# Performance work log

Hardware: AMD Instinct MI355X
Metric: run time of the kernel (lower is better)

The kernel has to match this reference:

```python
import jax, jax.numpy as jnp
import numpy as np

B, N, D, H, W, C = 2, 4, 48, 28, 60, 64
DOWNSAMPLE = 8
NX, NY, NZ = 192, 192, 1   # from size=(192,192), scale=0.25; zbound=[-10,10,20] -> nz=1
SCALE = 0.25
OFFSETX = 0
DMIN, DMAX, DSTEP = 2.0, 50.0, 1.0


def setup_inputs() -> dict:
    key = jax.random.key(0)
    x = jax.random.normal(key, (B, N, D, H, W, C), dtype=jnp.float32)
    ogfW, ogfH = W * DOWNSAMPLE, H * DOWNSAMPLE
    fx = fy = 250.0
    K = jnp.array([[fx, 0.0, ogfW / 2.0], [0.0, fy, ogfH / 2.0], [0.0, 0.0, 1.0]], jnp.float32)
    intrinsics = jnp.broadcast_to(K, (B, N, 3, 3))
    # camera->ego rotation: cam z (forward) -> ego x, cam x (right) -> ego -y, cam y (down) -> ego -z
    R = jnp.array([[0.0, 0.0, 1.0], [-1.0, 0.0, 0.0], [0.0, -1.0, 0.0]], jnp.float32)
    pose = jnp.zeros((B, N, 4, 4), jnp.float32)
    pose = pose.at[..., :3, :3].set(R)
    pose = pose.at[..., :3, 3].set(jnp.array([1.0, 0.0, 1.6], jnp.float32))
    pose = pose.at[..., 3, 3].set(1.0)
    return {"x": x, "intrinsics": intrinsics, "pose": pose}


def _frustum():
    # (D,H,W,3) frustum of (u*d, v*d, d) homogeneous pixel coords scaled by depth
    ds = jnp.arange(DMIN, DMAX, DSTEP, dtype=jnp.float32)          # (D,)
    xs = jnp.linspace(0.0, W * DOWNSAMPLE - 1, W, dtype=jnp.float32)
    ys = jnp.linspace(0.0, H * DOWNSAMPLE - 1, H, dtype=jnp.float32)
    d = jnp.broadcast_to(ds[:, None, None], (D, H, W))
    u = jnp.broadcast_to(xs[None, None, :], (D, H, W))
    v = jnp.broadcast_to(ys[None, :, None], (D, H, W))
    return jnp.stack([u * d, v * d, d], axis=-1)


def reference(x, intrinsics, pose):
    rots = pose[..., :3, :3]                 # (B,N,3,3)
    trans = pose[..., :3, 3]                 # (B,N,3)
    pts = _frustum()                         # (D,H,W,3)
    combine = rots @ jnp.linalg.inv(intrinsics)  # (B,N,3,3)
    # ego-frame point cloud: (B,N,D,H,W,3)
    geom = jnp.einsum('bnij,dhwj->bndhwi', combine, pts) + trans[:, :, None, None, None, :]
    # bev_intrinsics from bev_params_to_intrinsics(size, scale, offsetx)
    f_bev = 1.0 / SCALE
    cx_bev = NX / 2.0 + OFFSETX
    cy_bev = NY / 2.0
    # torch .long() truncates toward zero, same as astype(int32)
    gx = (geom[..., 0] * f_bev + cx_bev).astype(jnp.int32)
    gy = (geom[..., 1] * f_bev + cy_bev).astype(jnp.int32)
    gz = ((geom[..., 2] + 10.0) / 20.0).astype(jnp.int32)  # (z - bx2 + dx2/2)/dx2, bx2=0, dx2=20
    b = jnp.broadcast_to(jnp.arange(B, dtype=jnp.int32)[:, None, None, None, None], gx.shape)
    kept = (gx >= 0) & (gx < NX) & (gy >= 0) & (gy < NY) & (gz >= 0) & (gz < NZ)
    # segment scatter-add == sort + cumsum-diff + scatter-set (ranks unique after reduction)
    flat = ((b * NZ + gz) * NY + gy) * NX + gx
    flat = jnp.where(kept, flat, 0).reshape(-1)
    xf = jnp.where(kept[..., None], x, jnp.zeros((), x.dtype)).reshape(-1, C)
    out = jnp.zeros((B * NZ * NY * NX, C), x.dtype).at[flat].add(xf)
    out = out.reshape(B, NZ, NY, NX, C)
    # final[b, :, z, y, x] layout then cat(unbind(dim=2), dim=1) -> (B, NZ*C, NY, NX)
    return out.transpose(0, 1, 4, 2, 3).reshape(B, NZ * C, NY, NX)
```

## Files before the change

kernel.cpp:

```cpp
#include <hip/hip_runtime.h>

#define BB 2
#define NN 4
#define DD 48
#define HH 28
#define WW 60
#define CC 64
#define NXg 192
#define NYg 192
#define NZg 1
#define DOWNS 8

constexpr int PTS    = BB * NN * DD * HH * WW;
constexpr int NCELLS = BB * NZg * NYg * NXg;
constexpr int NYX    = NYg * NXg;

__global__ void setup_kernel(const float* __restrict__ intr,
                             const float* __restrict__ pose,
                             double* __restrict__ coef) {
    int i = threadIdx.x;
    if (i >= BB * NN) return;
    const float* K  = intr + (size_t)i * 9;
    const float* Pm = pose + (size_t)i * 16;

    double k00 = K[0], k01 = K[1], k02 = K[2];
    double k10 = K[3], k11 = K[4], k12 = K[5];
    double k20 = K[6], k21 = K[7], k22 = K[8];

    double det = k00 * (k11 * k22 - k12 * k21)
               - k01 * (k10 * k22 - k12 * k20)
               + k02 * (k10 * k21 - k11 * k20);
    double id = 1.0 / det;
    double i00 = (k11 * k22 - k12 * k21) * id;
    double i01 = (k02 * k21 - k01 * k22) * id;
    double i02 = (k01 * k12 - k02 * k11) * id;
    double i10 = (k12 * k20 - k10 * k22) * id;
    double i11 = (k00 * k22 - k02 * k20) * id;
    double i12 = (k02 * k10 - k00 * k12) * id;
    double i20 = (k10 * k21 - k11 * k20) * id;
    double i21 = (k01 * k20 - k00 * k21) * id;
    double i22 = (k00 * k11 - k01 * k10) * id;

    double r00 = Pm[0],  r01 = Pm[1],  r02 = Pm[2],  tx = Pm[3];
    double r10 = Pm[4],  r11 = Pm[5],  r12 = Pm[6],  ty = Pm[7];
    double r20 = Pm[8],  r21 = Pm[9],  r22 = Pm[10], tz = Pm[11];

    double* c = coef + (size_t)i * 12;
    c[0] = r00 * i00 + r01 * i10 + r02 * i20;
    c[1] = r00 * i01 + r01 * i11 + r02 * i21;
    c[2] = r00 * i02 + r01 * i12 + r02 * i22;
    c[3] = r10 * i00 + r11 * i10 + r12 * i20;
    c[4] = r10 * i01 + r11 * i11 + r12 * i21;
    c[5] = r10 * i02 + r11 * i12 + r12 * i22;
    c[6] = r20 * i00 + r21 * i10 + r22 * i20;
    c[7] = r20 * i01 + r21 * i11 + r22 * i21;
    c[8] = r20 * i02 + r21 * i12 + r22 * i22;
    c[9]  = tx;
    c[10] = ty;
    c[11] = tz;
}

__global__ void __launch_bounds__(256)
scatter_kernel(const float* __restrict__ x,
               const double* __restrict__ coef,
               float* __restrict__ outT) {
    int tid  = threadIdx.x;
    int lane = tid & 63;
    int p    = blockIdx.x * 256 + tid;

    int w  = p % WW;
    int t  = p / WW;
    int h  = t % HH; t /= HH;
    int d  = t % DD;
    int bn = t / DD;
    int b  = bn / NN;

    const double* cf = coef + (size_t)bn * 12;

    double u   = (double)w * ((double)(WW * DOWNS - 1) / (double)(WW - 1));
    double v   = (double)h * ((double)(HH * DOWNS - 1) / (double)(HH - 1));
    double dep = 2.0 + (double)d;

    double rx = cf[0] * u + cf[1] * v + cf[2];
    double ry = cf[3] * u + cf[4] * v + cf[5];
    double rz = cf[6] * u + cf[7] * v + cf[8];

    double gxf = (rx * dep + cf[9])  * 4.0 + 96.0;
    double gyf = (ry * dep + cf[10]) * 4.0 + 96.0;
    double gzf = ((rz * dep + cf[11]) + 10.0) / 20.0;

    int gx = (int)gxf;
    int gy = (int)gyf;
    int gz = (int)gzf;

    bool kept = (gx >= 0) & (gx < NXg) & (gy >= 0) & (gy < NYg) &
                (gz >= 0) & (gz < NZg);

    int cell = kept ? (((b * NZg + gz) * NYg + gy) * NXg + gx) : -1;

    unsigned long long mask = __ballot(cell >= 0);
    if (mask == 0ULL) return;

    int base = p - lane;
    float acc = 0.f;
    int   cur = -1;

    while (mask) {
        int k[8], c[8];
        #pragma unroll
        for (int j = 0; j < 8; ++j) {
            k[j] = __ffsll((long long)mask) - 1;
            mask &= mask - 1ULL;
        }
        #pragma unroll
        for (int j = 0; j < 8; ++j) {
            int kj = k[j] >= 0 ? k[j] : 0;
            int cj = __shfl(cell, kj);
            c[j] = k[j] >= 0 ? cj : -1;
        }
        float val[8];
        #pragma unroll
        for (int j = 0; j < 8; ++j) {
            int kj = k[j] >= 0 ? k[j] : 0;
            val[j] = x[(size_t)(base + kj) * CC + lane];
        }
        #pragma unroll
        for (int j = 0; j < 8; ++j) {
            if (c[j] < 0) continue;
            if (c[j] == cur) {
                acc += val[j];
            } else {
                if (cur >= 0) atomicAdd(&outT[(size_t)cur * CC + lane], acc);
                cur = c[j];
                acc = val[j];
            }
        }
    }
    if (cur >= 0) atomicAdd(&outT[(size_t)cur * CC + lane], acc);
}

__global__ void __launch_bounds__(256)
transpose_kernel(const float* __restrict__ outT,
                 float* __restrict__ out) {
    __shared__ float tile[64][65];
    int tid      = threadIdx.x;
    int cellbase = blockIdx.x * 64;

    const float* src = outT + (size_t)cellbase * CC;
    #pragma unroll
    for (int i = 0; i < 16; ++i) {
        int idx = i * 256 + tid;
        tile[idx >> 6][idx & 63] = src[idx];
    }
    __syncthreads();

    int bb     = cellbase / NYX;
    int yxbase = cellbase % NYX;
    float* dst = out + (size_t)bb * CC * NYX + yxbase;
    #pragma unroll
    for (int i = 0; i < 16; ++i) {
        int idx = i * 256 + tid;
        int ch  = idx >> 6;
        int cl  = idx & 63;
        dst[(size_t)ch * NYX + cl] = tile[cl][ch];
    }
}

extern "C" void kernel_launch(void* const* d_in, const int* in_sizes, int n_in,
                              void* d_out, int out_size, void* d_ws, size_t ws_size,
                              hipStream_t stream) {
    const float* x    = (const float*)d_in[0];
    const float* intr = (const float*)d_in[1];
    const float* pose = (const float*)d_in[2];
    float* out = (float*)d_out;

    double* coef = (double*)d_ws;
    float*  outT = (float*)d_ws + 256;

    hipMemsetAsync(outT, 0, (size_t)NCELLS * CC * sizeof(float), stream);
    setup_kernel<<<1, 64, 0, stream>>>(intr, pose, coef);
    scatter_kernel<<<PTS / 256, 256, 0, stream>>>(x, coef, outT);
    transpose_kernel<<<NCELLS / 64, 256, 0, stream>>>(outT, out);
}
```

Before: 270.6 us.

## Remap scatter so each wave reduces a full (b,d,w) column across cameras and rows

Result: faster. 229.2 us (-15.3%).

```diff
diff --git a/kernel.cpp b/kernel.cpp
--- a/kernel.cpp
+++ b/kernel.cpp
@@ -11,9 +11,10 @@
 #define NZg 1
 #define DOWNS 8
 
-constexpr int PTS    = BB * NN * DD * HH * WW;
+constexpr int DHW    = DD * HH * WW;
 constexpr int NCELLS = BB * NZg * NYg * NXg;
 constexpr int NYX    = NYg * NXg;
+constexpr int GWAVES = BB * DD * WW;
 
 __global__ void setup_kernel(const float* __restrict__ intr,
                              const float* __restrict__ pose,
@@ -66,73 +67,96 @@
                float* __restrict__ outT) {
     int tid  = threadIdx.x;
     int lane = tid & 63;
-    int p    = blockIdx.x * 256 + tid;
-
-    int w  = p % WW;
-    int t  = p / WW;
-    int h  = t % HH; t /= HH;
-    int d  = t % DD;
-    int bn = t / DD;
-    int b  = bn / NN;
-
-    const double* cf = coef + (size_t)bn * 12;
+    int gw   = blockIdx.x * 4 + (tid >> 6);
+
+    int w = gw % WW;
+    int t = gw / WW;
+    int d = t % DD;
+    int b = t / DD;
 
     double u   = (double)w * ((double)(WW * DOWNS - 1) / (double)(WW - 1));
-    double v   = (double)h * ((double)(HH * DOWNS - 1) / (double)(HH - 1));
     double dep = 2.0 + (double)d;
-
-    double rx = cf[0] * u + cf[1] * v + cf[2];
-    double ry = cf[3] * u + cf[4] * v + cf[5];
-    double rz = cf[6] * u + cf[7] * v + cf[8];
-
-    double gxf = (rx * dep + cf[9])  * 4.0 + 96.0;
-    double gyf = (ry * dep + cf[10]) * 4.0 + 96.0;
-    double gzf = ((rz * dep + cf[11]) + 10.0) / 20.0;
-
-    int gx = (int)gxf;
-    int gy = (int)gyf;
-    int gz = (int)gzf;
-
-    bool kept = (gx >= 0) & (gx < NXg) & (gy >= 0) & (gy < NYg) &
-                (gz >= 0) & (gz < NZg);
-
-    int cell = kept ? (((b * NZg + gz) * NYg + gy) * NXg + gx) : -1;
-
-    unsigned long long mask = __ballot(cell >= 0);
-    if (mask == 0ULL) return;
-
-    int base = p - lane;
+    const double vstep = (double)(HH * DOWNS - 1) / (double)(HH - 1);
+
+    int    cellv[4];
+    double Az[4], Bz[4];
+    bool   fastok = true;
+    #pragma unroll
+    for (int n = 0; n < NN; ++n) {
+        const double* cf = coef + (size_t)(b * NN + n) * 12;
+        double Bx = cf[1] * dep * 4.0;
+        double By = cf[4] * dep * 4.0;
+        if (Bx != 0.0 || By != 0.0) fastok = false;
+        double gxf = ((cf[0] * u + cf[2]) * dep + cf[9])  * 4.0 + 96.0;
+        double gyf = ((cf[3] * u + cf[5]) * dep + cf[10]) * 4.0 + 96.0;
+        int gx = (int)gxf;
+        int gy = (int)gyf;
+        bool kxy = (gx >= 0) & (gx < NXg) & (gy >= 0) & (gy < NYg);
+        cellv[n] = kxy ? ((b * NZg + 0) * NYg + gy) * NXg + gx : -1;
+        Az[n] = ((cf[6] * u + cf[8]) * dep + cf[11] + 10.0) / 20.0;
+        Bz[n] = cf[7] * dep * vstep / 20.0;
+    }
+    bool same = (cellv[0] == cellv[1]) & (cellv[1] == cellv[2]) &
+                (cellv[2] == cellv[3]);
+
+    unsigned hm[4];
+    #pragma unroll
+    for (int n = 0; n < NN; ++n) {
+        unsigned m = 0;
+        #pragma unroll
+        for (int h = 0; h < HH; ++h) {
+            double zf = Az[n] + Bz[n] * (double)h;
+            int gz = (int)zf;
+            m |= (gz == 0 ? 1u : 0u) << h;
+        }
+        hm[n] = m;
+    }
+    bool eqm = (hm[0] == hm[1]) & (hm[1] == hm[2]) & (hm[2] == hm[3]);
+
+    size_t xrow = ((size_t)(b * NN) * DHW + (size_t)d * HH * WW + w) * CC + lane;
+
+    if (fastok & same & eqm) {
+        if (cellv[0] < 0 || hm[0] == 0u) return;
+        unsigned m = hm[0];
+        float acc = 0.f;
+        #pragma unroll
+        for (int h = 0; h < HH; ++h) {
+            float s = ((m >> h) & 1u) ? 1.f : 0.f;
+            size_t r = xrow + (size_t)(h * WW) * CC;
+            float v0 = x[r + (size_t)(0 * DHW) * CC];
+            float v1 = x[r + (size_t)(1 * DHW) * CC];
+            float v2 = x[r + (size_t)(2 * DHW) * CC];
+            float v3 = x[r + (size_t)(3 * DHW) * CC];
+            acc += s * ((v0 + v1) + (v2 + v3));
+        }
+        atomicAdd(&outT[(size_t)cellv[0] * CC + lane], acc);
+        return;
+    }
+
     float acc = 0.f;
     int   cur = -1;
-
-    while (mask) {
-        int k[8], c[8];
-        #pragma unroll
-        for (int j = 0; j < 8; ++j) {
-            k[j] = __ffsll((long long)mask) - 1;
-            mask &= mask - 1ULL;
-        }
-        #pragma unroll
-        for (int j = 0; j < 8; ++j) {
-            int kj = k[j] >= 0 ? k[j] : 0;
-            int cj = __shfl(cell, kj);
-            c[j] = k[j] >= 0 ? cj : -1;
-        }
-        float val[8];
-        #pragma unroll
-        for (int j = 0; j < 8; ++j) {
-            int kj = k[j] >= 0 ? k[j] : 0;
-            val[j] = x[(size_t)(base + kj) * CC + lane];
-        }
-        #pragma unroll
-        for (int j = 0; j < 8; ++j) {
-            if (c[j] < 0) continue;
-            if (c[j] == cur) {
-                acc += val[j];
-            } else {
-                if (cur >= 0) atomicAdd(&outT[(size_t)cur * CC + lane], acc);
-                cur = c[j];
-                acc = val[j];
+    for (int n = 0; n < NN; ++n) {
+        const double* cf = coef + (size_t)(b * NN + n) * 12;
+        for (int h = 0; h < HH; ++h) {
+            double v = (double)h * vstep;
+            double gxf = ((cf[0] * u + cf[1] * v + cf[2]) * dep + cf[9])  * 4.0 + 96.0;
+            double gyf = ((cf[3] * u + cf[4] * v + cf[5]) * dep + cf[10]) * 4.0 + 96.0;
+            double gzf = ((cf[6] * u + cf[7] * v + cf[8]) * dep + cf[11] + 10.0) / 20.0;
+            int gx = (int)gxf;
+            int gy = (int)gyf;
+            int gz = (int)gzf;
+            bool kept = (gx >= 0) & (gx < NXg) & (gy >= 0) & (gy < NYg) &
+                        (gz >= 0) & (gz < NZg);
+            if (kept) {
+                int cell = ((b * NZg + gz) * NYg + gy) * NXg + gx;
+                float xv = x[xrow + (size_t)(n * DHW + h * WW) * CC];
+                if (cell == cur) {
+                    acc += xv;
+                } else {
+                    if (cur >= 0) atomicAdd(&outT[(size_t)cur * CC + lane], acc);
+                    cur = cell;
+                    acc = xv;
+                }
             }
         }
     }
@@ -179,6 +203,6 @@
 
     hipMemsetAsync(outT, 0, (size_t)NCELLS * CC * sizeof(float), stream);
     setup_kernel<<<1, 64, 0, stream>>>(intr, pose, coef);
-    scatter_kernel<<<PTS / 256, 256, 0, stream>>>(x, coef, outT);
+    scatter_kernel<<<GWAVES / 4, 256, 0, stream>>>(x, coef, outT);
     transpose_kernel<<<NCELLS / 64, 256, 0, stream>>>(outT, out);
 }
```
